# Optimization experiments

Measured on AMD Instinct MI355X. Metric: run time of the kernel, lower is better.

## Reference

```python
import jax, jax.numpy as jnp
import numpy as np

ITERATIONS = 5
B, N, M = 32, 2048, 2048


def vec2mat(trans):
    # trans: [B, 3] = [theta, tx, ty] -> [B, 3, 3] homogeneous transform
    c = jnp.cos(trans[:, 0])
    s = jnp.sin(trans[:, 0])
    tx, ty = trans[:, 1], trans[:, 2]
    z = jnp.zeros_like(c)
    o = jnp.ones_like(c)
    row0 = jnp.stack([c, -s, tx], axis=-1)
    row1 = jnp.stack([s, c, ty], axis=-1)
    row2 = jnp.stack([z, z, o], axis=-1)
    return jnp.stack([row0, row1, row2], axis=1)


def setup_inputs() -> dict:
    key = jax.random.key(0)
    k1, k2, k3 = jax.random.split(key, 3)
    source = jax.random.normal(k1, (B, N, 2), dtype=jnp.float32)
    target = jax.random.normal(k2, (B, M, 2), dtype=jnp.float32)
    init_transformation = jax.random.normal(k3, (B, 3), dtype=jnp.float32)
    return {"source": source, "target": target,
            "init_transformation": init_transformation}


def reference(source, target, init_transformation):
    T = vec2mat(init_transformation)  # [B,3,3]

    def apply_T(T):
        # equivalent to [source | 1] @ T^T, keeping xy columns
        R = T[:, :2, :2]
        t = T[:, :2, 2]
        return jnp.einsum('bnd,bed->bne', source, R) + t[:, None, :]

    st = apply_T(T)  # transformed source, [B,N,2]
    t_sq = jnp.sum(target ** 2, axis=-1)  # [B,M]

    for _ in range(ITERATIONS):
        # squared euclidean distances via ||s||^2 + ||t||^2 - 2 s.t (avoids [B,N,M,2])
        s_sq = jnp.sum(st ** 2, axis=-1)  # [B,N]
        cross = jnp.einsum('bnd,bmd->bnm', st, target)
        dists = s_sq[:, :, None] + t_sq[:, None, :] - 2.0 * cross  # [B,N,M]
        weights = jax.nn.softmax(-dists, axis=-1)
        target_corr = jnp.einsum('bnm,bmd->bnd', weights, target)  # [B,N,2]

        centroid_s = jnp.mean(st, axis=1, keepdims=True)          # [B,1,2]
        centroid_t = jnp.mean(target_corr, axis=1, keepdims=True)  # [B,1,2]
        H = jnp.einsum('bnd,bne->bde', st - centroid_s, target_corr - centroid_t)  # [B,2,2]

        U, S, Vh = jnp.linalg.svd(H, full_matrices=False)
        V = jnp.swapaxes(Vh, -1, -2)
        R_delta = V @ jnp.swapaxes(U, -1, -2)  # [B,2,2]
        t_delta = jnp.swapaxes(centroid_t, 1, 2) - R_delta @ jnp.swapaxes(centroid_s, 1, 2)  # [B,2,1]

        delta_theta = jnp.arctan2(R_delta[:, 1, 0], R_delta[:, 0, 0])
        delta_vec = jnp.stack([delta_theta, t_delta[:, 0, 0], t_delta[:, 1, 0]], axis=1)
        T = vec2mat(delta_vec) @ T
        st = apply_T(T)

    refined = jnp.stack([jnp.arctan2(T[:, 1, 0], T[:, 0, 0]),
                         T[:, 0, 2], T[:, 1, 2]], axis=1)
    return refined
```

## Files before the change

### kernel.cpp

```cpp
#include <hip/hip_runtime.h>
#include <math.h>

#define BN 32
#define NPTS 2048
#define MPTS 2048
#define ITERS 5
#define LOG2E 1.44269504088896340736f
#define SHIFT_C 14.0f

typedef _Float16 v8h __attribute__((ext_vector_type(8)));
typedef _Float16 v4h __attribute__((ext_vector_type(4)));
typedef __fp16   f16x2 __attribute__((ext_vector_type(2)));
typedef float    v4f __attribute__((ext_vector_type(4)));

#define TS_OFF   0
#define PART_OFF 2048

__device__ __forceinline__ void kabsch_compose(const float* a8,
                                               float& Tc, float& Ts,
                                               float& Ttx, float& Tty) {
    const float Ssx = a8[0], Ssy = a8[1], Stcx = a8[2], Stcy = a8[3];
    const float Sxx = a8[4], Sxy = a8[5], Syx = a8[6], Syy = a8[7];
    const float invN = 1.0f / (float)NPTS;
    const float csx = Ssx * invN, csy = Ssy * invN;
    const float ctx = Stcx * invN, cty = Stcy * invN;
    const float Hxx = Sxx - Ssx * ctx;
    const float Hxy = Sxy - Ssx * cty;
    const float Hyx = Syx - Ssy * ctx;
    const float Hyy = Syy - Ssy * cty;
    const float a = Hxx, bb = Hyx, cc = Hxy, d = Hyy;
    const float det = a * d - bb * cc;
    const bool refl = (det < 0.f);
    const float xr = refl ? (a - d) : (a + d);
    const float yr = refl ? (bb + cc) : (cc - bb);
    const float r = fmaxf(sqrtf(xr * xr + yr * yr), 1e-30f);
    const float R00 = xr / r, R10 = yr / r;
    const float R01 = refl ? R10 : -R10;
    const float R11 = refl ? -R00 : R00;
    const float tdx = ctx - (R00 * csx + R01 * csy);
    const float tdy = cty - (R10 * csx + R11 * csy);
    const float cD = R00, sD = R10;
    const float nC  = cD * Tc - sD * Ts;
    const float nS  = sD * Tc + cD * Ts;
    const float nTx = cD * Ttx - sD * Tty + tdx;
    const float nTy = sD * Ttx + cD * Tty + tdy;
    Tc = nC; Ts = nS; Ttx = nTx; Tty = nTy;
}

__global__ __launch_bounds__(512, 4) void icp_pass(const float* __restrict__ source,
                                                   const float* __restrict__ target,
                                                   const float* __restrict__ init_t,
                                                   float* __restrict__ ws,
                                                   int iter) {
    __shared__ v8h A1s[2050];
    __shared__ v8h A2s[516];
    __shared__ float4 comb[8][4][16];
    __shared__ float red[2][8];
    __shared__ float shT[6];
    __shared__ float pacc[128];
    const int tid = threadIdx.x;
    const int wv  = tid >> 6;
    const int l   = tid & 63;
    const int q   = l >> 4;
    const int col = l & 15;
    const int wq  = wv & 3;
    const int rg  = wv >> 2;
    const int b   = blockIdx.x & 31;
    const int gg  = blockIdx.x >> 5;
    const int g   = gg * 2 + rg;

    const _Float16 h0 = (_Float16)0.0f;
    const _Float16 h1 = (_Float16)1.0f;

    const float2* tg = (const float2*)target + b * MPTS;
#pragma unroll
    for (int i = 0; i < 4; ++i) {
        const int m = tid + i * 512;
        const float2 k = tg[m];
        const float bm = -LOG2E * fmaf(k.x, k.x, k.y * k.y);
        const _Float16 kxh = (_Float16)k.x;
        const _Float16 kxl = (_Float16)(k.x - (float)kxh);
        const _Float16 kyh = (_Float16)k.y;
        const _Float16 kyl = (_Float16)(k.y - (float)kyh);
        const _Float16 bmh = (_Float16)bm;
        const _Float16 bml = (_Float16)(bm - (float)bmh);
        A1s[m] = (v8h){kxh, kxh, kxl, kyh, kyh, kyl, bmh, bml};
    }
    if (tid < 512) {
        const int e = tid;
        const float2 k0 = tg[e * 4 + 0];
        const float2 k1 = tg[e * 4 + 1];
        const float2 k2 = tg[e * 4 + 2];
        const float2 k3 = tg[e * 4 + 3];
        A2s[e] = (v8h){(_Float16)k0.x, (_Float16)k1.x, (_Float16)k2.x, (_Float16)k3.x,
                       (_Float16)k0.y, (_Float16)k1.y, (_Float16)k2.y, (_Float16)k3.y};
    }
    if (tid == 0) {
        A1s[2048] = (v8h){h1, h1, h0, h0, h0, h0, h0, h0};
        A1s[2049] = (v8h){h0, h0, h0, h0, h0, h0, h0, h0};
        A2s[512]  = (v8h){h1, h1, h1, h1, h0, h0, h0, h0};
        A2s[513]  = (v8h){h0, h0, h0, h0, h0, h0, h0, h0};
    }

    if (iter == 0) {
        if (tid == 0) {
            const float th = init_t[b * 3 + 0];
            const float c = cosf(th), s = sinf(th);
            shT[0] = c; shT[1] = -s; shT[2] = init_t[b * 3 + 1];
            shT[3] = s; shT[4] = c;  shT[5] = init_t[b * 3 + 2];
            float* Tw = ws + TS_OFF + b * 6;
            Tw[0] = shT[0]; Tw[1] = shT[1]; Tw[2] = shT[2];
            Tw[3] = shT[3]; Tw[4] = shT[4]; Tw[5] = shT[5];
        }
    } else {
        if (tid < 128)
            pacc[tid] = ws[PART_OFF + (size_t)(iter - 1) * BN * 128 + b * 128 + tid];
        __syncthreads();
        if (tid == 0) {
            float a8[8];
#pragma unroll
            for (int j = 0; j < 8; ++j) {
                float s = 0.f;
#pragma unroll
                for (int s16 = 0; s16 < 16; ++s16) s += pacc[s16 * 8 + j];
                a8[j] = s;
            }
            const float* Tp = ws + TS_OFF + (iter - 1) * 192 + b * 6;
            float Tc = Tp[0], Ts = Tp[3], Ttx = Tp[2], Tty = Tp[5];
            kabsch_compose(a8, Tc, Ts, Ttx, Tty);
            shT[0] = Tc; shT[1] = -Ts; shT[2] = Ttx;
            shT[3] = Ts; shT[4] = Tc;  shT[5] = Tty;
            float* Tw = ws + TS_OFF + iter * 192 + b * 6;
            Tw[0] = Tc; Tw[1] = -Ts; Tw[2] = Ttx;
            Tw[3] = Ts; Tw[4] = Tc;  Tw[5] = Tty;
        }
    }
    __syncthreads();
    const float r00 = shT[0], r01 = shT[1], tx = shT[2];
    const float r10 = shT[3], r11 = shT[4], ty = shT[5];

    v8h B1[4];
#pragma unroll
    for (int nt = 0; nt < 4; ++nt) {
        const int row = g * 64 + nt * 16 + col;
        const float2 sp = ((const float2*)source)[b * NPTS + row];
        const float sx = fmaf(r00, sp.x, fmaf(r01, sp.y, tx));
        const float sy = fmaf(r10, sp.x, fmaf(r11, sp.y, ty));
        const float qpx = 2.0f * LOG2E * sx;
        const float qpy = 2.0f * LOG2E * sy;
        const float rc  = SHIFT_C - LOG2E * fmaf(sx, sx, sy * sy);
        const _Float16 qpxh = (_Float16)qpx;
        const _Float16 qpxl = (_Float16)(qpx - (float)qpxh);
        const _Float16 qpyh = (_Float16)qpy;
        const _Float16 qpyl = (_Float16)(qpy - (float)qpyh);
        const _Float16 rch  = (_Float16)rc;
        const _Float16 rcl  = (_Float16)(rc - (float)rch);
        v8h f;
        if (q == 0)      f = (v8h){qpxh, qpxl, qpxh, qpyh, qpyl, qpyh, h1, h1};
        else if (q == 1) f = (v8h){rch, rcl, h0, h0, h0, h0, h0, h0};
        else             f = (v8h){h0, h0, h0, h0, h0, h0, h0, h0};
        B1[nt] = f;
    }
    __syncthreads();

    const char* A1c = (const char*)A1s;
    const char* A2c = (const char*)A2s;
    int ad1 = (q == 0) ? (wq * 512 + col) * 16 : ((q == 1) ? 2048 * 16 : 2049 * 16);
    const int st1 = (q == 0) ? 256 : 0;
    int ad2 = (col == 1) ? (wq * 2048 + q * 16)
            : (col == 2) ? (wq * 2048 + q * 16 + 8)
            : ((col == 0) ? 512 * 16 : 513 * 16);
    const int st2 = (col == 1 || col == 2) ? 64 : 0;
    const v4f zero4 = (v4f){0.f, 0.f, 0.f, 0.f};

    v4f D2[4];
#pragma unroll
    for (int nt = 0; nt < 4; ++nt) D2[nt] = zero4;

    v8h a1w[32];
    v4h a2w[32];
    v4f D1w[32][4];
    a1w[0] = *(const v8h*)(A1c + ad1); a2w[0] = *(const v4h*)(A2c + ad2);
    ad1 += st1; ad2 += st2;
    a1w[1] = *(const v8h*)(A1c + ad1); a2w[1] = *(const v4h*)(A2c + ad2);
    ad1 += st1; ad2 += st2;
#pragma unroll
    for (int nt = 0; nt < 4; ++nt)
        D1w[0][nt] = __builtin_amdgcn_mfma_f32_16x16x32_f16(a1w[0], B1[nt], zero4, 0, 0, 0);

#pragma unroll
    for (int t = 0; t < 32; ++t) {
        if (t < 30) {
            a1w[t + 2] = *(const v8h*)(A1c + ad1);
            a2w[t + 2] = *(const v4h*)(A2c + ad2);
            ad1 += st1; ad2 += st2;
        }
        if (t < 31) {
#pragma unroll
            for (int nt = 0; nt < 4; ++nt)
                D1w[t + 1][nt] = __builtin_amdgcn_mfma_f32_16x16x32_f16(a1w[t + 1], B1[nt], zero4, 0, 0, 0);
        }
        float e[16];
#pragma unroll
        for (int nt = 0; nt < 4; ++nt)
#pragma unroll
            for (int j = 0; j < 4; ++j)
                e[nt * 4 + j] = __builtin_amdgcn_exp2f(D1w[t][nt][j]);
#pragma unroll
        for (int nt = 0; nt < 4; ++nt) {
            union { v4h v; f16x2 h[2]; } u;
            u.h[0] = __builtin_amdgcn_cvt_pkrtz(e[nt * 4 + 0], e[nt * 4 + 1]);
            u.h[1] = __builtin_amdgcn_cvt_pkrtz(e[nt * 4 + 2], e[nt * 4 + 3]);
            D2[nt] = __builtin_amdgcn_mfma_f32_16x16x16f16(a2w[t], u.v, D2[nt], 0, 0, 0);
        }
    }

    if (l < 16) {
#pragma unroll
        for (int nt = 0; nt < 4; ++nt)
            comb[wv][nt][col] = make_float4(D2[nt][0], D2[nt][1], D2[nt][2], 0.f);
    }
    __syncthreads();
    float den = 0.f, ax = 0.f, ay = 0.f;
#pragma unroll
    for (int w = 0; w < 4; ++w) {
        const float4 p = comb[rg * 4 + w][q][col];
        den += p.x; ax += p.y; ay += p.z;
    }
    const float tcx = ax / den;
    const float tcy = ay / den;
    const int erow = g * 64 + q * 16 + col;
    const float2 sp = ((const float2*)source)[b * NPTS + erow];
    const float sx = fmaf(r00, sp.x, fmaf(r01, sp.y, tx));
    const float sy = fmaf(r10, sp.x, fmaf(r11, sp.y, ty));
    float v[8] = {sx, sy, tcx, tcy, sx * tcx, sx * tcy, sy * tcx, sy * tcy};
#pragma unroll
    for (int off = 32; off > 0; off >>= 1) {
#pragma unroll
        for (int j = 0; j < 8; ++j) v[j] += __shfl_xor(v[j], off, 64);
    }
    if (l == 0 && wq == 0) {
#pragma unroll
        for (int j = 0; j < 8; ++j) red[rg][j] = v[j];
    }
    __syncthreads();
    if (tid < 2) {
        float4* slot = (float4*)(ws + PART_OFF + (size_t)iter * BN * 128 + b * 128 + gg * 8);
        slot[tid] = make_float4(red[0][tid * 4 + 0] + red[1][tid * 4 + 0],
                                red[0][tid * 4 + 1] + red[1][tid * 4 + 1],
                                red[0][tid * 4 + 2] + red[1][tid * 4 + 2],
                                red[0][tid * 4 + 3] + red[1][tid * 4 + 3]);
    }
}

__global__ __launch_bounds__(64) void icp_finish(float* __restrict__ out,
                                                 const float* __restrict__ ws) {
    const int b = threadIdx.x;
    if (b >= BN) return;
    const float* base = ws + PART_OFF + (size_t)(ITERS - 1) * BN * 128 + b * 128;
    float a8[8] = {0.f, 0.f, 0.f, 0.f, 0.f, 0.f, 0.f, 0.f};
    for (int s16 = 0; s16 < 16; ++s16)
#pragma unroll
        for (int j = 0; j < 8; ++j) a8[j] += base[s16 * 8 + j];
    const float* Tp = ws + TS_OFF + (ITERS - 1) * 192 + b * 6;
    float Tc = Tp[0], Ts = Tp[3], Ttx = Tp[2], Tty = Tp[5];
    kabsch_compose(a8, Tc, Ts, Ttx, Tty);
    out[b * 3 + 0] = atan2f(Ts, Tc);
    out[b * 3 + 1] = Ttx;
    out[b * 3 + 2] = Tty;
}

extern "C" void kernel_launch(void* const* d_in, const int* in_sizes, int n_in,
                              void* d_out, int out_size, void* d_ws, size_t ws_size,
                              hipStream_t stream) {
    const float* source = (const float*)d_in[0];
    const float* target = (const float*)d_in[1];
    const float* initt  = (const float*)d_in[2];
    float* out = (float*)d_out;
    float* ws  = (float*)d_ws;

    for (int k = 0; k < ITERS; ++k)
        icp_pass<<<BN * 16, 512, 0, stream>>>(source, target, initt, ws, k);
    icp_finish<<<1, 64, 0, stream>>>(out, ws);
}
```

Before: 157.1 us.

## Fuse ICP iterations into one persistent kernel with per-batch atomic barriers

Replaces the five per-iteration launches and the finish launch with one persistent kernel. Each block builds the target tables in LDS once and loops over iterations. The 16 blocks of a batch synchronise through a global atomic counter spin-wait, and every block then computes the Kabsch update redundantly. This removes launch overhead and the repeated per-pass LDS rebuilds, but adds a memset launch and spin-wait barriers that require all 512 blocks of a batch group to be co-resident.

Measured after the change: 591.2 us. 276% more time.

```diff
diff --git a/kernel.cpp b/kernel.cpp
--- a/kernel.cpp
+++ b/kernel.cpp
@@ -13,8 +13,7 @@
 typedef __fp16   f16x2 __attribute__((ext_vector_type(2)));
 typedef float    v4f __attribute__((ext_vector_type(4)));
 
-#define TS_OFF   0
-#define PART_OFF 2048
+#define PART_OFF 256
 
 __device__ __forceinline__ void kabsch_compose(const float* a8,
                                                float& Tc, float& Ts,
@@ -47,11 +46,11 @@
     Tc = nC; Ts = nS; Ttx = nTx; Tty = nTy;
 }
 
-__global__ __launch_bounds__(512, 4) void icp_pass(const float* __restrict__ source,
-                                                   const float* __restrict__ target,
-                                                   const float* __restrict__ init_t,
-                                                   float* __restrict__ ws,
-                                                   int iter) {
+__global__ __launch_bounds__(512, 4) void icp_persist(const float* __restrict__ source,
+                                                      const float* __restrict__ target,
+                                                      const float* __restrict__ init_t,
+                                                      float* __restrict__ out,
+                                                      float* __restrict__ ws) {
     __shared__ v8h A1s[2050];
     __shared__ v8h A2s[516];
     __shared__ float4 comb[8][4][16];
@@ -86,35 +85,161 @@
         const _Float16 bml = (_Float16)(bm - (float)bmh);
         A1s[m] = (v8h){kxh, kxh, kxl, kyh, kyh, kyl, bmh, bml};
     }
-    if (tid < 512) {
+    {
         const int e = tid;
-        const float2 k0 = tg[e * 4 + 0];
-        const float2 k1 = tg[e * 4 + 1];
-        const float2 k2 = tg[e * 4 + 2];
-        const float2 k3 = tg[e * 4 + 3];
-        A2s[e] = (v8h){(_Float16)k0.x, (_Float16)k1.x, (_Float16)k2.x, (_Float16)k3.x,
-                       (_Float16)k0.y, (_Float16)k1.y, (_Float16)k2.y, (_Float16)k3.y};
+        if (e < 512) {
+            const float2 k0 = tg[e * 4 + 0];
+            const float2 k1 = tg[e * 4 + 1];
+            const float2 k2 = tg[e * 4 + 2];
+            const float2 k3 = tg[e * 4 + 3];
+            A2s[e] = (v8h){(_Float16)k0.x, (_Float16)k1.x, (_Float16)k2.x, (_Float16)k3.x,
+                           (_Float16)k0.y, (_Float16)k1.y, (_Float16)k2.y, (_Float16)k3.y};
+        }
     }
     if (tid == 0) {
         A1s[2048] = (v8h){h1, h1, h0, h0, h0, h0, h0, h0};
         A1s[2049] = (v8h){h0, h0, h0, h0, h0, h0, h0, h0};
         A2s[512]  = (v8h){h1, h1, h1, h1, h0, h0, h0, h0};
         A2s[513]  = (v8h){h0, h0, h0, h0, h0, h0, h0, h0};
-    }
-
-    if (iter == 0) {
+        const float th = init_t[b * 3 + 0];
+        const float c = cosf(th), s = sinf(th);
+        shT[0] = c; shT[1] = -s; shT[2] = init_t[b * 3 + 1];
+        shT[3] = s; shT[4] = c;  shT[5] = init_t[b * 3 + 2];
+    }
+    __syncthreads();
+
+    const char* A1c = (const char*)A1s;
+    const char* A2c = (const char*)A2s;
+    const int ad1b = (q == 0) ? (wq * 512 + col) * 16 : ((q == 1) ? 2048 * 16 : 2049 * 16);
+    const int st1  = (q == 0) ? 256 : 0;
+    const int ad2b = (col == 1) ? (wq * 2048 + q * 16)
+                   : (col == 2) ? (wq * 2048 + q * 16 + 8)
+                   : ((col == 0) ? 512 * 16 : 513 * 16);
+    const int st2  = (col == 1 || col == 2) ? 64 : 0;
+    const v4f zero4 = (v4f){0.f, 0.f, 0.f, 0.f};
+
+    int* cnt = (int*)ws;
+
+    for (int iter = 0; iter < ITERS; ++iter) {
+        const float r00 = shT[0], r01 = shT[1], tx = shT[2];
+        const float r10 = shT[3], r11 = shT[4], ty = shT[5];
+
+        v8h B1[4];
+#pragma unroll
+        for (int nt = 0; nt < 4; ++nt) {
+            const int row = g * 64 + nt * 16 + col;
+            const float2 sp = ((const float2*)source)[b * NPTS + row];
+            const float sx = fmaf(r00, sp.x, fmaf(r01, sp.y, tx));
+            const float sy = fmaf(r10, sp.x, fmaf(r11, sp.y, ty));
+            const float qpx = 2.0f * LOG2E * sx;
+            const float qpy = 2.0f * LOG2E * sy;
+            const float rc  = SHIFT_C - LOG2E * fmaf(sx, sx, sy * sy);
+            const _Float16 qpxh = (_Float16)qpx;
+            const _Float16 qpxl = (_Float16)(qpx - (float)qpxh);
+            const _Float16 qpyh = (_Float16)qpy;
+            const _Float16 qpyl = (_Float16)(qpy - (float)qpyh);
+            const _Float16 rch  = (_Float16)rc;
+            const _Float16 rcl  = (_Float16)(rc - (float)rch);
+            v8h f;
+            if (q == 0)      f = (v8h){qpxh, qpxl, qpxh, qpyh, qpyl, qpyh, h1, h1};
+            else if (q == 1) f = (v8h){rch, rcl, h0, h0, h0, h0, h0, h0};
+            else             f = (v8h){h0, h0, h0, h0, h0, h0, h0, h0};
+            B1[nt] = f;
+        }
+
+        v4f D2[4];
+#pragma unroll
+        for (int nt = 0; nt < 4; ++nt) D2[nt] = zero4;
+
+        int ad1 = ad1b, ad2 = ad2b;
+        v8h a1w[32];
+        v4h a2w[32];
+        v4f D1w[32][4];
+        a1w[0] = *(const v8h*)(A1c + ad1); a2w[0] = *(const v4h*)(A2c + ad2);
+        ad1 += st1; ad2 += st2;
+        a1w[1] = *(const v8h*)(A1c + ad1); a2w[1] = *(const v4h*)(A2c + ad2);
+        ad1 += st1; ad2 += st2;
+#pragma unroll
+        for (int nt = 0; nt < 4; ++nt)
+            D1w[0][nt] = __builtin_amdgcn_mfma_f32_16x16x32_f16(a1w[0], B1[nt], zero4, 0, 0, 0);
+
+#pragma unroll
+        for (int t = 0; t < 32; ++t) {
+            if (t < 30) {
+                a1w[t + 2] = *(const v8h*)(A1c + ad1);
+                a2w[t + 2] = *(const v4h*)(A2c + ad2);
+                ad1 += st1; ad2 += st2;
+            }
+            if (t < 31) {
+#pragma unroll
+                for (int nt = 0; nt < 4; ++nt)
+                    D1w[t + 1][nt] = __builtin_amdgcn_mfma_f32_16x16x32_f16(a1w[t + 1], B1[nt], zero4, 0, 0, 0);
+            }
+            float e[16];
+#pragma unroll
+            for (int nt = 0; nt < 4; ++nt)
+#pragma unroll
+                for (int j = 0; j < 4; ++j)
+                    e[nt * 4 + j] = __builtin_amdgcn_exp2f(D1w[t][nt][j]);
+#pragma unroll
+            for (int nt = 0; nt < 4; ++nt) {
+                union { v4h v; f16x2 h[2]; } u;
+                u.h[0] = __builtin_amdgcn_cvt_pkrtz(e[nt * 4 + 0], e[nt * 4 + 1]);
+                u.h[1] = __builtin_amdgcn_cvt_pkrtz(e[nt * 4 + 2], e[nt * 4 + 3]);
+                D2[nt] = __builtin_amdgcn_mfma_f32_16x16x16f16(a2w[t], u.v, D2[nt], 0, 0, 0);
+            }
+        }
+
+        if (l < 16) {
+#pragma unroll
+            for (int nt = 0; nt < 4; ++nt)
+                comb[wv][nt][col] = make_float4(D2[nt][0], D2[nt][1], D2[nt][2], 0.f);
+        }
+        __syncthreads();
+        float den = 0.f, ax = 0.f, ay = 0.f;
+#pragma unroll
+        for (int w = 0; w < 4; ++w) {
+            const float4 p = comb[rg * 4 + w][q][col];
+            den += p.x; ax += p.y; ay += p.z;
+        }
+        const float tcx = ax / den;
+        const float tcy = ay / den;
+        const int erow = g * 64 + q * 16 + col;
+        const float2 sp = ((const float2*)source)[b * NPTS + erow];
+        const float sx = fmaf(r00, sp.x, fmaf(r01, sp.y, tx));
+        const float sy = fmaf(r10, sp.x, fmaf(r11, sp.y, ty));
+        float v[8] = {sx, sy, tcx, tcy, sx * tcx, sx * tcy, sy * tcx, sy * tcy};
+#pragma unroll
+        for (int off = 32; off > 0; off >>= 1) {
+#pragma unroll
+            for (int j = 0; j < 8; ++j) v[j] += __shfl_xor(v[j], off, 64);
+        }
+        if (l == 0 && wq == 0) {
+#pragma unroll
+            for (int j = 0; j < 8; ++j) red[rg][j] = v[j];
+        }
+        __syncthreads();
+
+        const int ci = iter * BN + b;
         if (tid == 0) {
-            const float th = init_t[b * 3 + 0];
-            const float c = cosf(th), s = sinf(th);
-            shT[0] = c; shT[1] = -s; shT[2] = init_t[b * 3 + 1];
-            shT[3] = s; shT[4] = c;  shT[5] = init_t[b * 3 + 2];
-            float* Tw = ws + TS_OFF + b * 6;
-            Tw[0] = shT[0]; Tw[1] = shT[1]; Tw[2] = shT[2];
-            Tw[3] = shT[3]; Tw[4] = shT[4]; Tw[5] = shT[5];
-        }
-    } else {
+            float* slot = ws + PART_OFF + ((size_t)(iter * BN + b) * 16 + gg) * 8;
+            float4* s4 = (float4*)slot;
+            s4[0] = make_float4(red[0][0] + red[1][0], red[0][1] + red[1][1],
+                                red[0][2] + red[1][2], red[0][3] + red[1][3]);
+            s4[1] = make_float4(red[0][4] + red[1][4], red[0][5] + red[1][5],
+                                red[0][6] + red[1][6], red[0][7] + red[1][7]);
+            __threadfence();
+            atomicAdd(&cnt[ci], 1);
+            while (__hip_atomic_load(&cnt[ci], __ATOMIC_RELAXED,
+                                     __HIP_MEMORY_SCOPE_AGENT) < 16) {
+                __builtin_amdgcn_s_sleep(8);
+            }
+        }
+        __syncthreads();
+        __threadfence();
+
         if (tid < 128)
-            pacc[tid] = ws[PART_OFF + (size_t)(iter - 1) * BN * 128 + b * 128 + tid];
+            pacc[tid] = ws[PART_OFF + ((size_t)(iter * BN + b) * 16) * 8 + tid];
         __syncthreads();
         if (tid == 0) {
             float a8[8];
@@ -125,149 +250,19 @@
                 for (int s16 = 0; s16 < 16; ++s16) s += pacc[s16 * 8 + j];
                 a8[j] = s;
             }
-            const float* Tp = ws + TS_OFF + (iter - 1) * 192 + b * 6;
-            float Tc = Tp[0], Ts = Tp[3], Ttx = Tp[2], Tty = Tp[5];
+            float Tc = shT[0], Ts = shT[3], Ttx = shT[2], Tty = shT[5];
             kabsch_compose(a8, Tc, Ts, Ttx, Tty);
             shT[0] = Tc; shT[1] = -Ts; shT[2] = Ttx;
             shT[3] = Ts; shT[4] = Tc;  shT[5] = Tty;
-            float* Tw = ws + TS_OFF + iter * 192 + b * 6;
-            Tw[0] = Tc; Tw[1] = -Ts; Tw[2] = Ttx;
-            Tw[3] = Ts; Tw[4] = Tc;  Tw[5] = Tty;
-        }
-    }
-    __syncthreads();
-    const float r00 = shT[0], r01 = shT[1], tx = shT[2];
-    const float r10 = shT[3], r11 = shT[4], ty = shT[5];
-
-    v8h B1[4];
-#pragma unroll
-    for (int nt = 0; nt < 4; ++nt) {
-        const int row = g * 64 + nt * 16 + col;
-        const float2 sp = ((const float2*)source)[b * NPTS + row];
-        const float sx = fmaf(r00, sp.x, fmaf(r01, sp.y, tx));
-        const float sy = fmaf(r10, sp.x, fmaf(r11, sp.y, ty));
-        const float qpx = 2.0f * LOG2E * sx;
-        const float qpy = 2.0f * LOG2E * sy;
-        const float rc  = SHIFT_C - LOG2E * fmaf(sx, sx, sy * sy);
-        const _Float16 qpxh = (_Float16)qpx;
-        const _Float16 qpxl = (_Float16)(qpx - (float)qpxh);
-        const _Float16 qpyh = (_Float16)qpy;
-        const _Float16 qpyl = (_Float16)(qpy - (float)qpyh);
-        const _Float16 rch  = (_Float16)rc;
-        const _Float16 rcl  = (_Float16)(rc - (float)rch);
-        v8h f;
-        if (q == 0)      f = (v8h){qpxh, qpxl, qpxh, qpyh, qpyl, qpyh, h1, h1};
-        else if (q == 1) f = (v8h){rch, rcl, h0, h0, h0, h0, h0, h0};
-        else             f = (v8h){h0, h0, h0, h0, h0, h0, h0, h0};
-        B1[nt] = f;
-    }
-    __syncthreads();
-
-    const char* A1c = (const char*)A1s;
-    const char* A2c = (const char*)A2s;
-    int ad1 = (q == 0) ? (wq * 512 + col) * 16 : ((q == 1) ? 2048 * 16 : 2049 * 16);
-    const int st1 = (q == 0) ? 256 : 0;
-    int ad2 = (col == 1) ? (wq * 2048 + q * 16)
-            : (col == 2) ? (wq * 2048 + q * 16 + 8)
-            : ((col == 0) ? 512 * 16 : 513 * 16);
-    const int st2 = (col == 1 || col == 2) ? 64 : 0;
-    const v4f zero4 = (v4f){0.f, 0.f, 0.f, 0.f};
-
-    v4f D2[4];
-#pragma unroll
-    for (int nt = 0; nt < 4; ++nt) D2[nt] = zero4;
-
-    v8h a1w[32];
-    v4h a2w[32];
-    v4f D1w[32][4];
-    a1w[0] = *(const v8h*)(A1c + ad1); a2w[0] = *(const v4h*)(A2c + ad2);
-    ad1 += st1; ad2 += st2;
-    a1w[1] = *(const v8h*)(A1c + ad1); a2w[1] = *(const v4h*)(A2c + ad2);
-    ad1 += st1; ad2 += st2;
-#pragma unroll
-    for (int nt = 0; nt < 4; ++nt)
-        D1w[0][nt] = __builtin_amdgcn_mfma_f32_16x16x32_f16(a1w[0], B1[nt], zero4, 0, 0, 0);
-
-#pragma unroll
-    for (int t = 0; t < 32; ++t) {
-        if (t < 30) {
-            a1w[t + 2] = *(const v8h*)(A1c + ad1);
-            a2w[t + 2] = *(const v4h*)(A2c + ad2);
-            ad1 += st1; ad2 += st2;
-        }
-        if (t < 31) {
-#pragma unroll
-            for (int nt = 0; nt < 4; ++nt)
-                D1w[t + 1][nt] = __builtin_amdgcn_mfma_f32_16x16x32_f16(a1w[t + 1], B1[nt], zero4, 0, 0, 0);
-        }
-        float e[16];
-#pragma unroll
-        for (int nt = 0; nt < 4; ++nt)
-#pragma unroll
-            for (int j = 0; j < 4; ++j)
-                e[nt * 4 + j] = __builtin_amdgcn_exp2f(D1w[t][nt][j]);
-#pragma unroll
-        for (int nt = 0; nt < 4; ++nt) {
-            union { v4h v; f16x2 h[2]; } u;
-            u.h[0] = __builtin_amdgcn_cvt_pkrtz(e[nt * 4 + 0], e[nt * 4 + 1]);
-            u.h[1] = __builtin_amdgcn_cvt_pkrtz(e[nt * 4 + 2], e[nt * 4 + 3]);
-            D2[nt] = __builtin_amdgcn_mfma_f32_16x16x16f16(a2w[t], u.v, D2[nt], 0, 0, 0);
-        }
-    }
-
-    if (l < 16) {
-#pragma unroll
-        for (int nt = 0; nt < 4; ++nt)
-            comb[wv][nt][col] = make_float4(D2[nt][0], D2[nt][1], D2[nt][2], 0.f);
-    }
-    __syncthreads();
-    float den = 0.f, ax = 0.f, ay = 0.f;
-#pragma unroll
-    for (int w = 0; w < 4; ++w) {
-        const float4 p = comb[rg * 4 + w][q][col];
-        den += p.x; ax += p.y; ay += p.z;
-    }
-    const float tcx = ax / den;
-    const float tcy = ay / den;
-    const int erow = g * 64 + q * 16 + col;
-    const float2 sp = ((const float2*)source)[b * NPTS + erow];
-    const float sx = fmaf(r00, sp.x, fmaf(r01, sp.y, tx));
-    const float sy = fmaf(r10, sp.x, fmaf(r11, sp.y, ty));
-    float v[8] = {sx, sy, tcx, tcy, sx * tcx, sx * tcy, sy * tcx, sy * tcy};
-#pragma unroll
-    for (int off = 32; off > 0; off >>= 1) {
-#pragma unroll
-        for (int j = 0; j < 8; ++j) v[j] += __shfl_xor(v[j], off, 64);
-    }
-    if (l == 0 && wq == 0) {
-#pragma unroll
-        for (int j = 0; j < 8; ++j) red[rg][j] = v[j];
-    }
-    __syncthreads();
-    if (tid < 2) {
-        float4* slot = (float4*)(ws + PART_OFF + (size_t)iter * BN * 128 + b * 128 + gg * 8);
-        slot[tid] = make_float4(red[0][tid * 4 + 0] + red[1][tid * 4 + 0],
-                                red[0][tid * 4 + 1] + red[1][tid * 4 + 1],
-                                red[0][tid * 4 + 2] + red[1][tid * 4 + 2],
-                                red[0][tid * 4 + 3] + red[1][tid * 4 + 3]);
-    }
-}
-
-__global__ __launch_bounds__(64) void icp_finish(float* __restrict__ out,
-                                                 const float* __restrict__ ws) {
-    const int b = threadIdx.x;
-    if (b >= BN) return;
-    const float* base = ws + PART_OFF + (size_t)(ITERS - 1) * BN * 128 + b * 128;
-    float a8[8] = {0.f, 0.f, 0.f, 0.f, 0.f, 0.f, 0.f, 0.f};
-    for (int s16 = 0; s16 < 16; ++s16)
-#pragma unroll
-        for (int j = 0; j < 8; ++j) a8[j] += base[s16 * 8 + j];
-    const float* Tp = ws + TS_OFF + (ITERS - 1) * 192 + b * 6;
-    float Tc = Tp[0], Ts = Tp[3], Ttx = Tp[2], Tty = Tp[5];
-    kabsch_compose(a8, Tc, Ts, Ttx, Tty);
-    out[b * 3 + 0] = atan2f(Ts, Tc);
-    out[b * 3 + 1] = Ttx;
-    out[b * 3 + 2] = Tty;
+        }
+        __syncthreads();
+    }
+
+    if (gg == 0 && tid == 0) {
+        out[b * 3 + 0] = atan2f(shT[3], shT[0]);
+        out[b * 3 + 1] = shT[2];
+        out[b * 3 + 2] = shT[5];
+    }
 }
 
 extern "C" void kernel_launch(void* const* d_in, const int* in_sizes, int n_in,
@@ -279,7 +274,6 @@
     float* out = (float*)d_out;
     float* ws  = (float*)d_ws;
 
-    for (int k = 0; k < ITERS; ++k)
-        icp_pass<<<BN * 16, 512, 0, stream>>>(source, target, initt, ws, k);
-    icp_finish<<<1, 64, 0, stream>>>(out, ws);
+    hipMemsetAsync(d_ws, 0, ITERS * BN * sizeof(int), stream);
+    icp_persist<<<BN * 16, 512, 0, stream>>>(source, target, initt, out, ws);
 }
```
